# Kernel tuning notes

Measured on AMD Instinct MI355X. Metric: run time of the kernel, lower is better.

Reference implementation:

```python
import jax, jax.numpy as jnp
import numpy as np

B, N, DIM = 8, 1024, 1024
HEADS, DIM_HEAD = 16, 64
INNER = HEADS * DIM_HEAD  # 1024
SCALE = DIM_HEAD ** -0.5


def setup_inputs() -> dict:
    key = jax.random.key(0)
    ks = jax.random.split(key, 7)
    x = jax.random.normal(ks[0], (B, N, DIM), dtype=jnp.float32)
    context = jax.random.normal(ks[1], (B, N, DIM), dtype=jnp.float32)
    lengths = jax.random.randint(ks[2], (B,), 1, N + 1, dtype=jnp.int32)
    # Linear weights stored as (in, out); scaled like torch default init
    Wq = jax.random.normal(ks[3], (DIM, INNER), dtype=jnp.float32) * (DIM ** -0.5)
    Wkv = jax.random.normal(ks[4], (DIM, 2 * INNER), dtype=jnp.float32) * (DIM ** -0.5)
    Wout = jax.random.normal(ks[5], (INNER, DIM), dtype=jnp.float32) * (INNER ** -0.5)
    bout = jnp.zeros((DIM,), dtype=jnp.float32)
    return {"x": x, "context": context, "lengths": lengths,
            "Wq": Wq, "Wkv": Wkv, "Wout": Wout, "bout": bout}


def reference(x, context, lengths, Wq, Wkv, Wout, bout):
    b, n, _ = x.shape
    h, d = HEADS, DIM_HEAD
    q = x @ Wq                       # [b, n, h*d]
    kv = context @ Wkv               # [b, n, 2*h*d]
    k, v = jnp.split(kv, 2, axis=-1)

    def split_heads(t):
        return t.reshape(b, n, h, d).transpose(0, 2, 1, 3)  # [b, h, n, d]

    q, k, v = split_heads(q), split_heads(k), split_heads(v)
    dots = jnp.einsum('bhid,bhjd->bhij', q, k) * SCALE       # [b, h, n, n]
    # mask over key axis j: valid where j < lengths[b]
    mask = jnp.arange(n)[None, :] < lengths[:, None]         # [b, n]
    mask_value = -jnp.finfo(dots.dtype).max
    dots = jnp.where(mask[:, None, None, :], dots, mask_value)
    attn = jax.nn.softmax(dots, axis=-1)
    out = jnp.einsum('bhij,bhjd->bhid', attn, v)             # [b, h, n, d]
    out = out.transpose(0, 2, 1, 3).reshape(b, n, h * d)     # [b, n, h*d]
    return out @ Wout + bout
```

## Files before the change

### kernel.cpp

```cpp
#include <hip/hip_runtime.h>
#include <hip/hip_bf16.h>
#include <math.h>

typedef __attribute__((ext_vector_type(4))) float f32x4;
typedef __attribute__((ext_vector_type(8))) short bf16x8;

#define DEVI __device__ __forceinline__
#define GLBP(p) ((const __attribute__((address_space(1))) void*)(p))
#define LDSP(p) ((__attribute__((address_space(3))) void*)(p))

DEVI unsigned short f2b(float x) {
    __hip_bfloat16 b = __float2bfloat16(x);
    return *reinterpret_cast<unsigned short*>(&b);
}

__global__ void cast_f32_to_bf16(const float* __restrict__ in,
                                 unsigned short* __restrict__ out, int n) {
    int stride = gridDim.x * blockDim.x;
    for (int i = blockIdx.x * blockDim.x + threadIdx.x; i * 4 < n; i += stride) {
        float4 v = reinterpret_cast<const float4*>(in)[i];
        ushort4 o;
        o.x = f2b(v.x); o.y = f2b(v.y); o.z = f2b(v.z); o.w = f2b(v.w);
        reinterpret_cast<ushort4*>(out)[i] = o;
    }
}

__global__ void transpose_cast(const float* __restrict__ in,
                               unsigned short* __restrict__ out, int R, int C) {
    __shared__ float t[32][33];
    int bc = blockIdx.x * 32, br = blockIdx.y * 32;
    int x = threadIdx.x, y = threadIdx.y;
#pragma unroll
    for (int j = 0; j < 32; j += 8)
        t[y + j][x] = in[(size_t)(br + y + j) * C + bc + x];
    __syncthreads();
#pragma unroll
    for (int j = 0; j < 32; j += 8)
        out[(size_t)(bc + y + j) * R + br + x] = f2b(t[x][y + j]);
}

template<int OUTF32>
__global__ __launch_bounds__(256, 2)
void gemm_bt(const unsigned short* __restrict__ A,
             const unsigned short* __restrict__ B,
             void* __restrict__ Cp, const float* __restrict__ bias,
             int M, int N, int K) {
    __shared__ unsigned short As[128 * 32];
    __shared__ unsigned short Bs[128 * 32];
    const int tid  = threadIdx.x;
    const int wave = tid >> 6;
    const int lane = tid & 63;
    const int nbn  = N >> 7;
    const int bm   = blockIdx.x / nbn;
    const int bn   = blockIdx.x - bm * nbn;

    const int lr  = lane & 15;
    const int lk8 = (lane >> 4) << 3;
    const int wr  = (wave >> 1) * 64;
    const int wc  = (wave & 1) * 64;

    const unsigned short* ag = A + (size_t)(bm * 128 + (tid >> 2)) * K + ((tid & 3) << 3);
    const unsigned short* bg = B + (size_t)(bn * 128 + (tid >> 2)) * K + ((tid & 3) << 3);
    unsigned short* asd = As + wave * 512;
    unsigned short* bsd = Bs + wave * 512;

    f32x4 acc[4][4];
#pragma unroll
    for (int m = 0; m < 4; ++m)
#pragma unroll
        for (int n = 0; n < 4; ++n)
            acc[m][n] = (f32x4){0.f, 0.f, 0.f, 0.f};

    for (int k0 = 0; k0 < K; k0 += 32) {
        __builtin_amdgcn_global_load_lds(GLBP(ag + k0),                    LDSP(asd),        16, 0, 0);
        __builtin_amdgcn_global_load_lds(GLBP(ag + (size_t)64 * K + k0),   LDSP(asd + 2048), 16, 0, 0);
        __builtin_amdgcn_global_load_lds(GLBP(bg + k0),                    LDSP(bsd),        16, 0, 0);
        __builtin_amdgcn_global_load_lds(GLBP(bg + (size_t)64 * K + k0),   LDSP(bsd + 2048), 16, 0, 0);
        __syncthreads();
        bf16x8 af[4], bfr[4];
#pragma unroll
        for (int m = 0; m < 4; ++m)
            af[m] = *reinterpret_cast<const bf16x8*>(&As[(wr + m * 16 + lr) * 32 + lk8]);
#pragma unroll
        for (int n = 0; n < 4; ++n)
            bfr[n] = *reinterpret_cast<const bf16x8*>(&Bs[(wc + n * 16 + lr) * 32 + lk8]);
#pragma unroll
        for (int m = 0; m < 4; ++m)
#pragma unroll
            for (int n = 0; n < 4; ++n)
                acc[m][n] = __builtin_amdgcn_mfma_f32_16x16x32_bf16(af[m], bfr[n], acc[m][n], 0, 0, 0);
        __syncthreads();
    }

    const int rb = (lane >> 4) << 2;
    if (OUTF32) {
        float* C = reinterpret_cast<float*>(Cp);
#pragma unroll
        for (int m = 0; m < 4; ++m)
#pragma unroll
            for (int n = 0; n < 4; ++n) {
                const int col = bn * 128 + wc + n * 16 + lr;
                const float bv = bias[col];
#pragma unroll
                for (int r = 0; r < 4; ++r) {
                    const int row = bm * 128 + wr + m * 16 + rb + r;
                    C[(size_t)row * N + col] = acc[m][n][r] + bv;
                }
            }
    } else {
        unsigned short* C = reinterpret_cast<unsigned short*>(Cp);
#pragma unroll
        for (int m = 0; m < 4; ++m)
#pragma unroll
            for (int n = 0; n < 4; ++n) {
                const int col = bn * 128 + wc + n * 16 + lr;
#pragma unroll
                for (int r = 0; r < 4; ++r) {
                    const int row = bm * 128 + wr + m * 16 + rb + r;
                    C[(size_t)row * N + col] = f2b(acc[m][n][r]);
                }
            }
    }
}

__global__ __launch_bounds__(256, 2)
void attn_fused(const unsigned short* __restrict__ Q,
                const unsigned short* __restrict__ KV,
                const int* __restrict__ lengths,
                unsigned short* __restrict__ O) {
    __shared__ unsigned short Vt[64 * 72];
    __shared__ unsigned short Pl[4][16 * 72];

    const int tid  = threadIdx.x;
    const int wave = tid >> 6;
    const int lane = tid & 63;
    const int bid = blockIdx.x;
    const int h  = ((bid >> 6) & 1) * 8 + (bid & 7);
    const int b  = (bid >> 3) & 7;
    const int qt = bid >> 7;
    const int L  = lengths[b];

    const int lr  = lane & 15;
    const int g   = lane >> 4;
    const int lk8 = g << 3;
    const int rb  = g << 2;

    const size_t kvbase = (size_t)(b * 1024) * 2048 + h * 64;

    const size_t qrow = (size_t)(b * 1024 + qt * 64 + wave * 16 + lr);
    bf16x8 qf[2];
    qf[0] = *reinterpret_cast<const bf16x8*>(&Q[qrow * 1024 + h * 64 + lk8]);
    qf[1] = *reinterpret_cast<const bf16x8*>(&Q[qrow * 1024 + h * 64 + 32 + lk8]);

    f32x4 oacc[4];
#pragma unroll
    for (int nd = 0; nd < 4; ++nd) oacc[nd] = (f32x4){0.f, 0.f, 0.f, 0.f};
    float mrun[4] = {-3.0e38f, -3.0e38f, -3.0e38f, -3.0e38f};
    float lrun[4] = {0.f, 0.f, 0.f, 0.f};

    const int ntiles = (L + 63) >> 6;
    for (int t = 0; t < ntiles; ++t) {
        const int j0 = t * 64;
        __syncthreads();

        bf16x8 vv[2];
#pragma unroll
        for (int rep = 0; rep < 2; ++rep) {
            const int dseg = ((rep * 4 + wave) & 7) << 3;
            vv[rep] = *reinterpret_cast<const bf16x8*>(
                &KV[kvbase + (size_t)(j0 + lane) * 2048 + 1024 + dseg]);
        }

        f32x4 sacc[4];
#pragma unroll
        for (int n = 0; n < 4; ++n) sacc[n] = (f32x4){0.f, 0.f, 0.f, 0.f};
#pragma unroll
        for (int n = 0; n < 4; ++n) {
            const unsigned short* kp = &KV[kvbase + (size_t)(j0 + n * 16 + lr) * 2048 + lk8];
            bf16x8 kf0 = *reinterpret_cast<const bf16x8*>(kp);
            bf16x8 kf1 = *reinterpret_cast<const bf16x8*>(kp + 32);
            sacc[n] = __builtin_amdgcn_mfma_f32_16x16x32_bf16(qf[0], kf0, sacc[n], 0, 0, 0);
            sacc[n] = __builtin_amdgcn_mfma_f32_16x16x32_bf16(qf[1], kf1, sacc[n], 0, 0, 0);
        }

#pragma unroll
        for (int rep = 0; rep < 2; ++rep) {
            const int dseg = ((rep * 4 + wave) & 7) << 3;
#pragma unroll
            for (int j = 0; j < 8; ++j)
                Vt[(dseg + j) * 72 + lane] = (unsigned short)vv[rep][j];
        }

        float sv[4][4];
#pragma unroll
        for (int n = 0; n < 4; ++n)
#pragma unroll
            for (int r = 0; r < 4; ++r) {
                const int key = j0 + n * 16 + lr;
                sv[n][r] = (key < L) ? sacc[n][r] * 0.125f : -3.0e38f;
            }

        float alpha[4], psum[4];
#pragma unroll
        for (int r = 0; r < 4; ++r) {
            float tm = fmaxf(fmaxf(sv[0][r], sv[1][r]), fmaxf(sv[2][r], sv[3][r]));
#pragma unroll
            for (int off = 1; off < 16; off <<= 1)
                tm = fmaxf(tm, __shfl_xor(tm, off));
            const float mn = fmaxf(mrun[r], tm);
            alpha[r] = __expf(mrun[r] - mn);
            mrun[r] = mn;
            psum[r] = 0.f;
        }
        float pv[4][4];
#pragma unroll
        for (int n = 0; n < 4; ++n)
#pragma unroll
            for (int r = 0; r < 4; ++r) {
                const float p = __expf(sv[n][r] - mrun[r]);
                pv[n][r] = p;
                psum[r] += p;
            }
#pragma unroll
        for (int r = 0; r < 4; ++r) {
#pragma unroll
            for (int off = 1; off < 16; off <<= 1)
                psum[r] += __shfl_xor(psum[r], off);
            lrun[r] = lrun[r] * alpha[r] + psum[r];
        }
#pragma unroll
        for (int nd = 0; nd < 4; ++nd)
#pragma unroll
            for (int r = 0; r < 4; ++r)
                oacc[nd][r] *= alpha[r];

#pragma unroll
        for (int n = 0; n < 4; ++n)
#pragma unroll
            for (int r = 0; r < 4; ++r)
                Pl[wave][(rb + r) * 72 + n * 16 + lr] = f2b(pv[n][r]);

        __syncthreads();

        bf16x8 pf0 = *reinterpret_cast<const bf16x8*>(&Pl[wave][lr * 72 + lk8]);
        bf16x8 pf1 = *reinterpret_cast<const bf16x8*>(&Pl[wave][lr * 72 + 32 + lk8]);
#pragma unroll
        for (int nd = 0; nd < 4; ++nd) {
            bf16x8 vf0 = *reinterpret_cast<const bf16x8*>(&Vt[(nd * 16 + lr) * 72 + lk8]);
            bf16x8 vf1 = *reinterpret_cast<const bf16x8*>(&Vt[(nd * 16 + lr) * 72 + 32 + lk8]);
            oacc[nd] = __builtin_amdgcn_mfma_f32_16x16x32_bf16(pf0, vf0, oacc[nd], 0, 0, 0);
            oacc[nd] = __builtin_amdgcn_mfma_f32_16x16x32_bf16(pf1, vf1, oacc[nd], 0, 0, 0);
        }
    }

    const size_t orow = (size_t)(b * 1024 + qt * 64 + wave * 16);
#pragma unroll
    for (int r = 0; r < 4; ++r) {
        const float inv = 1.0f / lrun[r];
#pragma unroll
        for (int nd = 0; nd < 4; ++nd)
            O[(orow + rb + r) * 1024 + h * 64 + nd * 16 + lr] = f2b(oacc[nd][r] * inv);
    }
}

extern "C" void kernel_launch(void* const* d_in, const int* in_sizes, int n_in,
                              void* d_out, int out_size, void* d_ws, size_t ws_size,
                              hipStream_t stream) {
    const float* x    = (const float*)d_in[0];
    const float* ctx  = (const float*)d_in[1];
    const int*   len  = (const int*)d_in[2];
    const float* Wq   = (const float*)d_in[3];
    const float* Wkv  = (const float*)d_in[4];
    const float* Wout = (const float*)d_in[5];
    const float* bout = (const float*)d_in[6];
    float* out = (float*)d_out;

    char* w = (char*)d_ws;
    unsigned short* xb   = (unsigned short*)w; w += (size_t)8192 * 1024 * 2;
    unsigned short* cb   = (unsigned short*)w; w += (size_t)8192 * 1024 * 2;
    unsigned short* qb   = (unsigned short*)w; w += (size_t)8192 * 1024 * 2;
    unsigned short* kvb  = (unsigned short*)w; w += (size_t)8192 * 2048 * 2;
    unsigned short* aob  = (unsigned short*)w; w += (size_t)8192 * 1024 * 2;
    unsigned short* wqt  = (unsigned short*)w; w += (size_t)1024 * 1024 * 2;
    unsigned short* wkvt = (unsigned short*)w; w += (size_t)2048 * 1024 * 2;
    unsigned short* wot  = (unsigned short*)w; w += (size_t)1024 * 1024 * 2;

    cast_f32_to_bf16<<<2048, 256, 0, stream>>>(x,   xb, 8192 * 1024);
    cast_f32_to_bf16<<<2048, 256, 0, stream>>>(ctx, cb, 8192 * 1024);
    dim3 tb(32, 8);
    transpose_cast<<<dim3(32, 32), tb, 0, stream>>>(Wq,   wqt,  1024, 1024);
    transpose_cast<<<dim3(64, 32), tb, 0, stream>>>(Wkv,  wkvt, 1024, 2048);
    transpose_cast<<<dim3(32, 32), tb, 0, stream>>>(Wout, wot,  1024, 1024);

    gemm_bt<0><<<512,  256, 0, stream>>>(xb, wqt,  (void*)qb,  nullptr, 8192, 1024, 1024);
    gemm_bt<0><<<1024, 256, 0, stream>>>(cb, wkvt, (void*)kvb, nullptr, 8192, 2048, 1024);
    attn_fused<<<2048, 256, 0, stream>>>(qb, kvb, len, aob);
    gemm_bt<1><<<512,  256, 0, stream>>>(aob, wot, (void*)out, bout, 8192, 1024, 1024);
}
```

Before: 371.8 us.

## Stage K/V tiles in LDS with register prefetch and swizzled V transpose

The attention kernel now loads each 64-key K/V tile with coalesced per-thread 16-byte loads and stages both K and transposed V in shared memory. The next tile's K/V is prefetched into registers while the current tile is computed, which overlaps global latency with MFMA and softmax work. V is written to LDS with a rotating column swizzle to reduce bank conflicts, and the per-wave barrier before the P·V step is dropped. Launch bounds rise to 4 blocks per CU, which caps registers per thread and may cause spilling, and the extra LDS buffer raises shared-memory use per block.

Result: faster. 349.0 us (-6.1%).

```diff
diff --git a/kernel.cpp b/kernel.cpp
--- a/kernel.cpp
+++ b/kernel.cpp
@@ -123,11 +123,12 @@
     }
 }
 
-__global__ __launch_bounds__(256, 2)
+__global__ __launch_bounds__(256, 4)
 void attn_fused(const unsigned short* __restrict__ Q,
                 const unsigned short* __restrict__ KV,
                 const int* __restrict__ lengths,
                 unsigned short* __restrict__ O) {
+    __shared__ unsigned short Kl[64 * 72];
     __shared__ unsigned short Vt[64 * 72];
     __shared__ unsigned short Pl[4][16 * 72];
 
@@ -145,6 +146,11 @@
     const int lk8 = g << 3;
     const int rb  = g << 2;
 
+    const int skey = tid >> 3;
+    const int sds  = (tid & 7) << 3;
+    const int vcol0 = (skey + sds) & 63;
+    const int vcol1 = (skey + 32 + sds) & 63;
+
     const size_t kvbase = (size_t)(b * 1024) * 2048 + h * 64;
 
     const size_t qrow = (size_t)(b * 1024 + qt * 64 + wave * 16 + lr);
@@ -159,36 +165,54 @@
     float lrun[4] = {0.f, 0.f, 0.f, 0.f};
 
     const int ntiles = (L + 63) >> 6;
+
+    bf16x8 kreg[2], vreg[2];
+    {
+        const size_t r0 = kvbase + (size_t)(skey)      * 2048 + sds;
+        const size_t r1 = kvbase + (size_t)(skey + 32) * 2048 + sds;
+        kreg[0] = *reinterpret_cast<const bf16x8*>(&KV[r0]);
+        kreg[1] = *reinterpret_cast<const bf16x8*>(&KV[r1]);
+        vreg[0] = *reinterpret_cast<const bf16x8*>(&KV[r0 + 1024]);
+        vreg[1] = *reinterpret_cast<const bf16x8*>(&KV[r1 + 1024]);
+    }
+
     for (int t = 0; t < ntiles; ++t) {
+        __syncthreads();
+
+        *reinterpret_cast<bf16x8*>(&Kl[skey * 72 + sds])        = kreg[0];
+        *reinterpret_cast<bf16x8*>(&Kl[(skey + 32) * 72 + sds]) = kreg[1];
+#pragma unroll
+        for (int j = 0; j < 8; ++j)
+            Vt[(sds + j) * 72 + vcol0] = (unsigned short)vreg[0][j];
+#pragma unroll
+        for (int j = 0; j < 8; ++j)
+            Vt[(sds + j) * 72 + vcol1] = (unsigned short)vreg[1][j];
+
+        {
+            const int j0n = (t + 1) * 64;
+            int r0i = j0n + skey;        r0i = r0i > 1023 ? 1023 : r0i;
+            int r1i = j0n + skey + 32;   r1i = r1i > 1023 ? 1023 : r1i;
+            const size_t r0 = kvbase + (size_t)r0i * 2048 + sds;
+            const size_t r1 = kvbase + (size_t)r1i * 2048 + sds;
+            kreg[0] = *reinterpret_cast<const bf16x8*>(&KV[r0]);
+            kreg[1] = *reinterpret_cast<const bf16x8*>(&KV[r1]);
+            vreg[0] = *reinterpret_cast<const bf16x8*>(&KV[r0 + 1024]);
+            vreg[1] = *reinterpret_cast<const bf16x8*>(&KV[r1 + 1024]);
+        }
+
+        __syncthreads();
+
         const int j0 = t * 64;
-        __syncthreads();
-
-        bf16x8 vv[2];
-#pragma unroll
-        for (int rep = 0; rep < 2; ++rep) {
-            const int dseg = ((rep * 4 + wave) & 7) << 3;
-            vv[rep] = *reinterpret_cast<const bf16x8*>(
-                &KV[kvbase + (size_t)(j0 + lane) * 2048 + 1024 + dseg]);
-        }
 
         f32x4 sacc[4];
 #pragma unroll
         for (int n = 0; n < 4; ++n) sacc[n] = (f32x4){0.f, 0.f, 0.f, 0.f};
 #pragma unroll
         for (int n = 0; n < 4; ++n) {
-            const unsigned short* kp = &KV[kvbase + (size_t)(j0 + n * 16 + lr) * 2048 + lk8];
-            bf16x8 kf0 = *reinterpret_cast<const bf16x8*>(kp);
-            bf16x8 kf1 = *reinterpret_cast<const bf16x8*>(kp + 32);
+            bf16x8 kf0 = *reinterpret_cast<const bf16x8*>(&Kl[(n * 16 + lr) * 72 + lk8]);
+            bf16x8 kf1 = *reinterpret_cast<const bf16x8*>(&Kl[(n * 16 + lr) * 72 + 32 + lk8]);
             sacc[n] = __builtin_amdgcn_mfma_f32_16x16x32_bf16(qf[0], kf0, sacc[n], 0, 0, 0);
             sacc[n] = __builtin_amdgcn_mfma_f32_16x16x32_bf16(qf[1], kf1, sacc[n], 0, 0, 0);
-        }
-
-#pragma unroll
-        for (int rep = 0; rep < 2; ++rep) {
-            const int dseg = ((rep * 4 + wave) & 7) << 3;
-#pragma unroll
-            for (int j = 0; j < 8; ++j)
-                Vt[(dseg + j) * 72 + lane] = (unsigned short)vv[rep][j];
         }
 
         float sv[4][4];
@@ -240,14 +264,15 @@
             for (int r = 0; r < 4; ++r)
                 Pl[wave][(rb + r) * 72 + n * 16 + lr] = f2b(pv[n][r]);
 
-        __syncthreads();
-
         bf16x8 pf0 = *reinterpret_cast<const bf16x8*>(&Pl[wave][lr * 72 + lk8]);
         bf16x8 pf1 = *reinterpret_cast<const bf16x8*>(&Pl[wave][lr * 72 + 32 + lk8]);
 #pragma unroll
         for (int nd = 0; nd < 4; ++nd) {
-            bf16x8 vf0 = *reinterpret_cast<const bf16x8*>(&Vt[(nd * 16 + lr) * 72 + lk8]);
-            bf16x8 vf1 = *reinterpret_cast<const bf16x8*>(&Vt[(nd * 16 + lr) * 72 + 32 + lk8]);
+            const int d = nd * 16 + lr;
+            const int c0 = (lk8 + (d & 56)) & 63;
+            const int c1 = ((32 + lk8) + (d & 56)) & 63;
+            bf16x8 vf0 = *reinterpret_cast<const bf16x8*>(&Vt[d * 72 + c0]);
+            bf16x8 vf1 = *reinterpret_cast<const bf16x8*>(&Vt[d * 72 + c1]);
             oacc[nd] = __builtin_amdgcn_mfma_f32_16x16x32_bf16(pf0, vf0, oacc[nd], 0, 0, 0);
             oacc[nd] = __builtin_amdgcn_mfma_f32_16x16x32_bf16(pf1, vf1, oacc[nd], 0, 0, 0);
         }
```
